# Kernel optimization log

Hardware: AMD Instinct MI355X
Metric: run time of the kernel (lower is better)

Reference implementation:

```python
import math
import jax, jax.numpy as jnp
import numpy as np

N_HEADS = 16
NUM_BUCKETS = 32
MAX_DISTANCE = 128


def _relative_position_bucket(relative_positions, num_buckets=NUM_BUCKETS, max_distance=MAX_DISTANCE):
    # bidirectional=True branch of the torch helper
    ret = -relative_positions
    nb = num_buckets // 2
    sign = (ret < 0).astype(jnp.int32)
    ret = jnp.abs(ret)
    max_exact = nb // 2
    is_small = ret < max_exact
    # torch .long() truncates toward zero; values in the selected (large) branch are >= 0 so int cast matches
    large = max_exact + jnp.minimum(
        (jnp.log(ret.astype(jnp.float32) / max_exact + 1e-6)
         / math.log(max_distance / max_exact) * (nb - max_exact)).astype(jnp.int32),
        nb - max_exact - 1,
    )
    return jnp.where(is_small, ret, large) + sign * nb


def setup_inputs() -> dict:
    key = jax.random.key(0)
    k1, k2, k3, k4, k5 = jax.random.split(key, 5)
    d_model = 1024
    B, L = 2, 2048
    return {
        "query": jax.random.normal(k1, (B, L, d_model), dtype=jnp.float32),
        "Wq": jax.random.normal(k2, (d_model, d_model), dtype=jnp.float32) * 0.02,
        "Wkv": jax.random.normal(k3, (d_model, 2 * d_model), dtype=jnp.float32) * 0.02,
        "Wo": jax.random.normal(k4, (d_model, d_model), dtype=jnp.float32) * 0.02,
        "rel_bias": jax.random.normal(k5, (N_HEADS * NUM_BUCKETS, 1), dtype=jnp.float32) * 0.02,
    }


def reference(query, Wq, Wkv, Wo, rel_bias):
    B, L, D = query.shape
    H = N_HEADS
    hd = D // H
    scale = 1.0 / math.sqrt(hd)

    q = query @ Wq                      # [B, L, D]
    kv = query @ Wkv                    # [B, L, 2D]
    k, v = jnp.split(kv, 2, axis=-1)

    def split_heads(x):
        return x.reshape(B, L, H, hd).transpose(0, 2, 1, 3)  # [B, H, L, hd]

    q, k, v = map(split_heads, (q, k, v))

    scores = jnp.einsum("bhqd,bhkd->bhqk", q, k) * scale      # [B, H, L, L]

    # relative position bias
    pos = jnp.arange(L)
    rp = pos[None, :] - pos[:, None]                           # mem - ctx, [L, L]
    buckets = _relative_position_bucket(rp)                    # [L, L]
    idx = buckets[None, :, :] + (jnp.arange(H) * NUM_BUCKETS)[:, None, None]  # [H, L, L]
    bias = rel_bias[idx, 0][None]                              # [1, H, L, L]

    attn = jax.nn.softmax(scores + bias, axis=-1)
    out = jnp.einsum("bhqk,bhkd->bhqd", attn, v)               # [B, H, L, hd]
    out = out.transpose(0, 2, 1, 3).reshape(B, L, D) @ Wo      # [B, L, D]
    return out, bias
```

## Files before the change

### kernel.cpp

```cpp
#include <hip/hip_runtime.h>


typedef unsigned short u16;
typedef unsigned int u32;
typedef __attribute__((ext_vector_type(4))) float f32x4;
typedef __attribute__((ext_vector_type(8))) short bf16x8;
typedef __attribute__((ext_vector_type(4))) unsigned short u16x4;

#define MFMA16(a, b, c) __builtin_amdgcn_mfma_f32_16x16x32_bf16(a, b, c, 0, 0, 0)

static __device__ inline u16 f2bf(float f) {
    u32 x = __float_as_uint(f);
    x += 0x7fffu + ((x >> 16) & 1u);
    return (u16)(x >> 16);
}
static __device__ inline u32 pk2(float a, float b) {
    return (u32)f2bf(a) | ((u32)f2bf(b) << 16);
}

__global__ __launch_bounds__(256) void build_table(
    const float* __restrict__ rel_bias, float* __restrict__ tbl)
{
    int i = blockIdx.x * 256 + threadIdx.x;
    if (i >= 16 * 4096) return;
    int rel = (i & 4095) - 2047;
    int h = i >> 12;
    int ret = -rel;
    int sign = (ret < 0) ? 1 : 0;
    int aret = (ret < 0) ? -ret : ret;
    int bucket;
    if (aret < 8) {
        bucket = aret;
    } else {
        float v = (logf((float)aret * 0.125f + 1e-6f) / logf(16.0f)) * 8.0f;
        int iv = (int)v;
        bucket = 8 + (iv < 7 ? iv : 7);
    }
    bucket += sign * 16;
    tbl[i] = rel_bias[h * 32 + bucket];
}

__global__ __launch_bounds__(256) void bias_fill(
    const float* __restrict__ tbl, float* __restrict__ out)
{
    const int bx = blockIdx.x;
    const int h = bx >> 11, i = bx & 2047;
    const float* tp = tbl + h * 4096 + 2047 - i;
    float* dst = out + 4194304 + ((size_t)bx << 11);
    const int j0 = threadIdx.x * 8;
    float4 v0, v1;
    v0.x = tp[j0 + 0]; v0.y = tp[j0 + 1]; v0.z = tp[j0 + 2]; v0.w = tp[j0 + 3];
    v1.x = tp[j0 + 4]; v1.y = tp[j0 + 5]; v1.z = tp[j0 + 6]; v1.w = tp[j0 + 7];
    float4* dv = (float4*)(dst + j0);
    dv[0] = v0; dv[1] = v1;
}

__global__ __launch_bounds__(256) void qkv_gemm(
    const float* __restrict__ X, const float* __restrict__ Wq,
    const float* __restrict__ Wkv, u16* __restrict__ qws,
    u16* __restrict__ kws, u16* __restrict__ vtws)
{
    __shared__ u16 As[128 * 40];
    __shared__ u16 Bs[128 * 40];
    const int tid = threadIdx.x;
    const int n0 = blockIdx.x * 128;
    const int m0 = blockIdx.y * 128;
    const float* Bw; int ldb, bn0;
    if (blockIdx.x < 8) { Bw = Wq;  ldb = 1024; bn0 = n0; }
    else                { Bw = Wkv; ldb = 2048; bn0 = n0 - 1024; }
    const int wid = tid >> 6, lane = tid & 63, c = lane & 15, quad = lane >> 4;
    const int wm = (wid >> 1) * 64, wn = (wid & 1) * 64;
    const f32x4 z = {0.f, 0.f, 0.f, 0.f};
    f32x4 acc[4][4];
    for (int i = 0; i < 4; i++) for (int j = 0; j < 4; j++) acc[i][j] = z;
    const int ar = tid >> 1, ac = (tid & 1) * 16;
    const int bkr = (tid >> 5) * 4, bnn = (tid & 31) * 4;

    for (int kk = 0; kk < 1024; kk += 32) {
        const float4* asrc = (const float4*)(X + (size_t)(m0 + ar) * 1024 + kk + ac);
        float4 a0 = asrc[0], a1 = asrc[1], a2 = asrc[2], a3 = asrc[3];
        const float* bbase = Bw + (size_t)(kk + bkr) * ldb + bn0 + bnn;
        float4 b0 = *(const float4*)(bbase);
        float4 b1 = *(const float4*)(bbase + ldb);
        float4 b2 = *(const float4*)(bbase + 2 * ldb);
        float4 b3 = *(const float4*)(bbase + 3 * ldb);
        uint4 w0 = { pk2(a0.x, a0.y), pk2(a0.z, a0.w), pk2(a1.x, a1.y), pk2(a1.z, a1.w) };
        uint4 w1 = { pk2(a2.x, a2.y), pk2(a2.z, a2.w), pk2(a3.x, a3.y), pk2(a3.z, a3.w) };
        *(uint4*)&As[ar * 40 + ac] = w0;
        *(uint4*)&As[ar * 40 + ac + 8] = w1;
        uint2 t0 = { pk2(b0.x, b1.x), pk2(b2.x, b3.x) };
        uint2 t1 = { pk2(b0.y, b1.y), pk2(b2.y, b3.y) };
        uint2 t2 = { pk2(b0.z, b1.z), pk2(b2.z, b3.z) };
        uint2 t3 = { pk2(b0.w, b1.w), pk2(b2.w, b3.w) };
        *(uint2*)&Bs[(bnn + 0) * 40 + bkr] = t0;
        *(uint2*)&Bs[(bnn + 1) * 40 + bkr] = t1;
        *(uint2*)&Bs[(bnn + 2) * 40 + bkr] = t2;
        *(uint2*)&Bs[(bnn + 3) * 40 + bkr] = t3;
        __syncthreads();
        bf16x8 af[4], bfr[4];
        for (int im = 0; im < 4; im++)
            af[im] = *(const bf16x8*)&As[(wm + im * 16 + c) * 40 + quad * 8];
        for (int jn = 0; jn < 4; jn++)
            bfr[jn] = *(const bf16x8*)&Bs[(wn + jn * 16 + c) * 40 + quad * 8];
        for (int im = 0; im < 4; im++)
            for (int jn = 0; jn < 4; jn++)
                acc[im][jn] = MFMA16(af[im], bfr[jn], acc[im][jn]);
        __syncthreads();
    }
    for (int im = 0; im < 4; im++) for (int jn = 0; jn < 4; jn++) {
        int gm0 = m0 + wm + im * 16 + quad * 4;
        int gn = n0 + wn + jn * 16 + c;
        if (gn < 2048) {
            u16* dstbase = (gn < 1024) ? qws : kws;
            int nn = gn & 1023;
            int h = nn >> 6, d = nn & 63;
            for (int r = 0; r < 4; r++) {
                int gm = gm0 + r, bb = gm >> 11, l = gm & 2047;
                dstbase[(((size_t)bb * 16 + h) * 2048 + l) * 64 + d] = f2bf(acc[im][jn][r]);
            }
        } else {
            int nn = gn - 2048;
            int h = nn >> 6, d = nn & 63;
            int bb = gm0 >> 11, l = gm0 & 2047;
            u16x4 pk = { f2bf(acc[im][jn][0]), f2bf(acc[im][jn][1]),
                         f2bf(acc[im][jn][2]), f2bf(acc[im][jn][3]) };
            *(u16x4*)&vtws[(((size_t)bb * 16 + h) * 64 + d) * 2048 + l] = pk;
        }
    }
}

__global__ __launch_bounds__(256) void attn_kernel(
    const u16* __restrict__ qws, const u16* __restrict__ kws,
    const u16* __restrict__ vtws, const float* __restrict__ tbl,
    u16* __restrict__ ows)
{
    __shared__ u16 Qs[128 * 72];
    __shared__ u16 Ks[64 * 72];
    __shared__ u16 Vt[64 * 72];
    __shared__ u16 Ps[4][32 * 72];
    const int tid = threadIdx.x;
    const int qt = blockIdx.x, bh = blockIdx.y;
    const int b = bh >> 4, h = bh & 15;
    const u16* qp = qws + (size_t)bh * 2048 * 64;
    const u16* kp = kws + (size_t)bh * 2048 * 64;
    const u16* vp = vtws + (size_t)bh * 64 * 2048;
    const float* tb = tbl + h * 4096;
    const int q0 = qt * 128;
    const int wid = tid >> 6, lane = tid & 63, c = lane & 15, quad = lane >> 4;

    {
        int row = tid >> 1, c0 = (tid & 1) * 32;
        const uint4* s = (const uint4*)(qp + (size_t)(q0 + row) * 64 + c0);
        uint4 v0 = s[0], v1 = s[1], v2 = s[2], v3 = s[3];
        uint4* d = (uint4*)&Qs[row * 72 + c0];
        d[0] = v0; d[1] = v1; d[2] = v2; d[3] = v3;
    }
    __syncthreads();
    const int qw0 = wid * 32;
    bf16x8 bq[2][2];
    for (int nt = 0; nt < 2; nt++)
        for (int ks = 0; ks < 2; ks++)
            bq[nt][ks] = *(const bf16x8*)&Qs[(qw0 + nt * 16 + c) * 72 + ks * 32 + quad * 8];

    float mrow[2] = { -__builtin_inff(), -__builtin_inff() };
    float lrow[2] = { 0.f, 0.f };
    const f32x4 z = {0.f, 0.f, 0.f, 0.f};
    f32x4 accO[2][4];
    for (int i = 0; i < 2; i++) for (int j = 0; j < 4; j++) accO[i][j] = z;
    const int srow = tid >> 2, sc0 = (tid & 3) * 16;

    for (int kt = 0; kt < 32; kt++) {
        const int k0 = kt * 64;
        __syncthreads();
        {
            const uint4* s1 = (const uint4*)(kp + (size_t)(k0 + srow) * 64 + sc0);
            uint4 x0 = s1[0], x1 = s1[1];
            const uint4* s2 = (const uint4*)(vp + (size_t)srow * 2048 + k0 + sc0);
            uint4 y0 = s2[0], y1 = s2[1];
            uint4* d1 = (uint4*)&Ks[srow * 72 + sc0]; d1[0] = x0; d1[1] = x1;
            uint4* d2 = (uint4*)&Vt[srow * 72 + sc0]; d2[0] = y0; d2[1] = y1;
        }
        __syncthreads();
        f32x4 accS[4][2];
        for (int i = 0; i < 4; i++) { accS[i][0] = z; accS[i][1] = z; }
        for (int ks = 0; ks < 2; ks++) {
            for (int ktile = 0; ktile < 4; ktile++) {
                bf16x8 ak = *(const bf16x8*)&Ks[(ktile * 16 + c) * 72 + ks * 32 + quad * 8];
                accS[ktile][0] = MFMA16(ak, bq[0][ks], accS[ktile][0]);
                accS[ktile][1] = MFMA16(ak, bq[1][ks], accS[ktile][1]);
            }
        }
        float sv[4][2][4];
        float tmax[2] = { -__builtin_inff(), -__builtin_inff() };
        for (int ktile = 0; ktile < 4; ktile++)
            for (int nt = 0; nt < 2; nt++) {
                int keyb = k0 + ktile * 16 + quad * 4;
                int qg = q0 + qw0 + nt * 16 + c;
                const float* tp = tb + (keyb - qg + 2047);
                for (int r = 0; r < 4; r++) {
                    float x = accS[ktile][nt][r] * 0.125f + tp[r];
                    sv[ktile][nt][r] = x;
                    tmax[nt] = fmaxf(tmax[nt], x);
                }
            }
        for (int nt = 0; nt < 2; nt++) {
            tmax[nt] = fmaxf(tmax[nt], __shfl_xor(tmax[nt], 16, 64));
            tmax[nt] = fmaxf(tmax[nt], __shfl_xor(tmax[nt], 32, 64));
        }
        float alpha[2], rsum[2] = { 0.f, 0.f };
        for (int nt = 0; nt < 2; nt++) {
            float mnew = fmaxf(mrow[nt], tmax[nt]);
            alpha[nt] = __expf(mrow[nt] - mnew);
            mrow[nt] = mnew;
        }
        for (int ktile = 0; ktile < 4; ktile++)
            for (int nt = 0; nt < 2; nt++) {
                float p0 = __expf(sv[ktile][nt][0] - mrow[nt]);
                float p1 = __expf(sv[ktile][nt][1] - mrow[nt]);
                float p2 = __expf(sv[ktile][nt][2] - mrow[nt]);
                float p3 = __expf(sv[ktile][nt][3] - mrow[nt]);
                rsum[nt] += (p0 + p1) + (p2 + p3);
                u16x4 pk = { f2bf(p0), f2bf(p1), f2bf(p2), f2bf(p3) };
                *(u16x4*)&Ps[wid][(nt * 16 + c) * 72 + ktile * 16 + quad * 4] = pk;
            }
        for (int nt = 0; nt < 2; nt++) {
            rsum[nt] += __shfl_xor(rsum[nt], 16, 64);
            rsum[nt] += __shfl_xor(rsum[nt], 32, 64);
            lrow[nt] = lrow[nt] * alpha[nt] + rsum[nt];
        }
        for (int mt = 0; mt < 2; mt++)
            for (int r = 0; r < 4; r++) {
                float aO = __shfl(alpha[mt], quad * 4 + r, 64);
                for (int nt = 0; nt < 4; nt++) accO[mt][nt][r] *= aO;
            }
        for (int kb = 0; kb < 2; kb++) {
            bf16x8 bv[4];
            for (int nt = 0; nt < 4; nt++)
                bv[nt] = *(const bf16x8*)&Vt[(nt * 16 + c) * 72 + kb * 32 + quad * 8];
            for (int mt = 0; mt < 2; mt++) {
                bf16x8 ap = *(const bf16x8*)&Ps[wid][(mt * 16 + c) * 72 + kb * 32 + quad * 8];
                for (int nt = 0; nt < 4; nt++)
                    accO[mt][nt] = MFMA16(ap, bv[nt], accO[mt][nt]);
            }
        }
    }
    for (int mt = 0; mt < 2; mt++)
        for (int r = 0; r < 4; r++) {
            float lq = __shfl(lrow[mt], quad * 4 + r, 64);
            float rl = 1.0f / lq;
            int qg = q0 + qw0 + mt * 16 + quad * 4 + r;
            size_t base = ((size_t)b * 2048 + qg) * 1024 + h * 64;
            for (int nt = 0; nt < 4; nt++)
                ows[base + nt * 16 + c] = f2bf(accO[mt][nt][r] * rl);
        }
}

__global__ __launch_bounds__(256) void out_gemm(
    const u16* __restrict__ O, const float* __restrict__ Wo, float* __restrict__ out)
{
    __shared__ u16 As[128 * 40];
    __shared__ u16 Bs[128 * 40];
    const int tid = threadIdx.x;
    const int n0 = blockIdx.x * 128;
    const int m0 = blockIdx.y * 128;
    const int wid = tid >> 6, lane = tid & 63, c = lane & 15, quad = lane >> 4;
    const int wm = (wid >> 1) * 64, wn = (wid & 1) * 64;
    const f32x4 z = {0.f, 0.f, 0.f, 0.f};
    f32x4 acc[4][4];
    for (int i = 0; i < 4; i++) for (int j = 0; j < 4; j++) acc[i][j] = z;
    const int ar = tid >> 1, ac = (tid & 1) * 16;
    const int bkr = (tid >> 5) * 4, bnn = (tid & 31) * 4;
    for (int kk = 0; kk < 1024; kk += 32) {
        const uint4* asrc = (const uint4*)(O + (size_t)(m0 + ar) * 1024 + kk + ac);
        uint4 a0 = asrc[0], a1 = asrc[1];
        const float* bbase = Wo + (size_t)(kk + bkr) * 1024 + n0 + bnn;
        float4 b0 = *(const float4*)(bbase);
        float4 b1 = *(const float4*)(bbase + 1024);
        float4 b2 = *(const float4*)(bbase + 2048);
        float4 b3 = *(const float4*)(bbase + 3072);
        *(uint4*)&As[ar * 40 + ac] = a0;
        *(uint4*)&As[ar * 40 + ac + 8] = a1;
        uint2 t0 = { pk2(b0.x, b1.x), pk2(b2.x, b3.x) };
        uint2 t1 = { pk2(b0.y, b1.y), pk2(b2.y, b3.y) };
        uint2 t2 = { pk2(b0.z, b1.z), pk2(b2.z, b3.z) };
        uint2 t3 = { pk2(b0.w, b1.w), pk2(b2.w, b3.w) };
        *(uint2*)&Bs[(bnn + 0) * 40 + bkr] = t0;
        *(uint2*)&Bs[(bnn + 1) * 40 + bkr] = t1;
        *(uint2*)&Bs[(bnn + 2) * 40 + bkr] = t2;
        *(uint2*)&Bs[(bnn + 3) * 40 + bkr] = t3;
        __syncthreads();
        bf16x8 af[4], bfr[4];
        for (int im = 0; im < 4; im++)
            af[im] = *(const bf16x8*)&As[(wm + im * 16 + c) * 40 + quad * 8];
        for (int jn = 0; jn < 4; jn++)
            bfr[jn] = *(const bf16x8*)&Bs[(wn + jn * 16 + c) * 40 + quad * 8];
        for (int im = 0; im < 4; im++)
            for (int jn = 0; jn < 4; jn++)
                acc[im][jn] = MFMA16(af[im], bfr[jn], acc[im][jn]);
        __syncthreads();
    }
    for (int im = 0; im < 4; im++) for (int jn = 0; jn < 4; jn++) {
        int gm0 = m0 + wm + im * 16 + quad * 4;
        int gn = n0 + wn + jn * 16 + c;
        for (int r = 0; r < 4; r++)
            out[(size_t)(gm0 + r) * 1024 + gn] = acc[im][jn][r];
    }
}

extern "C" void kernel_launch(void* const* d_in, const int* in_sizes, int n_in,
                              void* d_out, int out_size, void* d_ws, size_t ws_size,
                              hipStream_t stream)
{
    (void)in_sizes; (void)n_in; (void)out_size; (void)ws_size;
    const float* query    = (const float*)d_in[0];
    const float* Wq       = (const float*)d_in[1];
    const float* Wkv      = (const float*)d_in[2];
    const float* Wo       = (const float*)d_in[3];
    const float* rel_bias = (const float*)d_in[4];
    float* out = (float*)d_out;

    float* tbl = (float*)d_ws;
    u16* qws  = (u16*)((char*)d_ws + 262144);
    u16* kws  = qws + 4194304;
    u16* vtws = kws + 4194304;
    u16* ows  = vtws + 4194304;

    build_table<<<256, 256, 0, stream>>>(rel_bias, tbl);
    bias_fill<<<32768, 256, 0, stream>>>(tbl, out);
    qkv_gemm<<<dim3(24, 32), 256, 0, stream>>>(query, Wq, Wkv, qws, kws, vtws);
    attn_kernel<<<dim3(16, 32), 256, 0, stream>>>(qws, kws, vtws, tbl, ows);
    out_gemm<<<dim3(8, 32), 256, 0, stream>>>(ows, Wo, out);
}
```

Measured before the change: 492.8 us.

## Pre-convert inputs to bf16, double-buffer attention K/V, drop online softmax rescaling

Adds pre-pass kernels that convert the activations to bf16 and transpose and convert all weights to bf16 K-major layout. Both GEMMs then load bf16 tiles directly with a 64-wide K step instead of converting fp32 inside the main loop. The attention kernel double-buffers K/V and a bias window in shared memory, prefetching the next tile during compute. It also removes the running-max softmax rescaling by exponentiating raw scores, which risks overflow for large logits.

```diff
diff --git a/kernel.cpp b/kernel.cpp
--- a/kernel.cpp
+++ b/kernel.cpp
@@ -40,6 +40,46 @@
     tbl[i] = rel_bias[h * 32 + bucket];
 }
 
+__global__ __launch_bounds__(256) void convert_x(
+    const float* __restrict__ X, u16* __restrict__ Xb)
+{
+    int i = (blockIdx.x * 256 + threadIdx.x) * 8;
+    float4 a = *(const float4*)(X + i);
+    float4 b = *(const float4*)(X + i + 4);
+    uint4 w = { pk2(a.x, a.y), pk2(a.z, a.w), pk2(b.x, b.y), pk2(b.z, b.w) };
+    *(uint4*)(Xb + i) = w;
+}
+
+__global__ __launch_bounds__(256) void transpose_w(
+    const float* __restrict__ Wq, const float* __restrict__ Wkv,
+    const float* __restrict__ Wo, u16* __restrict__ Wt)
+{
+    __shared__ u16 T[64 * 72];
+    const int tid = threadIdx.x;
+    const int k0 = blockIdx.x * 64;
+    const int nt = blockIdx.y;
+    const int n0 = nt * 64;
+    const float* src; int ld, nb;
+    if (n0 < 1024)      { src = Wq;  ld = 1024; nb = n0; }
+    else if (n0 < 3072) { src = Wkv; ld = 2048; nb = n0 - 1024; }
+    else                { src = Wo;  ld = 1024; nb = n0 - 3072; }
+    const int r0 = tid >> 4, c4 = (tid & 15) * 4;
+    for (int rr = 0; rr < 4; rr++) {
+        int row = rr * 16 + r0;
+        float4 f = *(const float4*)(src + (size_t)(k0 + row) * ld + nb + c4);
+        T[(c4 + 0) * 72 + row] = f2bf(f.x);
+        T[(c4 + 1) * 72 + row] = f2bf(f.y);
+        T[(c4 + 2) * 72 + row] = f2bf(f.z);
+        T[(c4 + 3) * 72 + row] = f2bf(f.w);
+    }
+    __syncthreads();
+    const int n = tid >> 2, ks0 = (tid & 3) * 16;
+    uint4 u0 = *(const uint4*)&T[n * 72 + ks0];
+    uint4 u1 = *(const uint4*)&T[n * 72 + ks0 + 8];
+    uint4* d = (uint4*)(Wt + (size_t)(n0 + n) * 1024 + k0 + ks0);
+    d[0] = u0; d[1] = u1;
+}
+
 __global__ __launch_bounds__(256) void bias_fill(
     const float* __restrict__ tbl, float* __restrict__ out)
 {
@@ -56,55 +96,47 @@
 }
 
 __global__ __launch_bounds__(256) void qkv_gemm(
-    const float* __restrict__ X, const float* __restrict__ Wq,
-    const float* __restrict__ Wkv, u16* __restrict__ qws,
-    u16* __restrict__ kws, u16* __restrict__ vtws)
-{
-    __shared__ u16 As[128 * 40];
-    __shared__ u16 Bs[128 * 40];
+    const u16* __restrict__ Xb, const u16* __restrict__ Wt,
+    u16* __restrict__ qws, u16* __restrict__ kws, u16* __restrict__ vtws)
+{
+    __shared__ u16 As[128 * 72];
+    __shared__ u16 Bs[128 * 72];
     const int tid = threadIdx.x;
     const int n0 = blockIdx.x * 128;
     const int m0 = blockIdx.y * 128;
-    const float* Bw; int ldb, bn0;
-    if (blockIdx.x < 8) { Bw = Wq;  ldb = 1024; bn0 = n0; }
-    else                { Bw = Wkv; ldb = 2048; bn0 = n0 - 1024; }
     const int wid = tid >> 6, lane = tid & 63, c = lane & 15, quad = lane >> 4;
     const int wm = (wid >> 1) * 64, wn = (wid & 1) * 64;
     const f32x4 z = {0.f, 0.f, 0.f, 0.f};
     f32x4 acc[4][4];
     for (int i = 0; i < 4; i++) for (int j = 0; j < 4; j++) acc[i][j] = z;
-    const int ar = tid >> 1, ac = (tid & 1) * 16;
-    const int bkr = (tid >> 5) * 4, bnn = (tid & 31) * 4;
-
-    for (int kk = 0; kk < 1024; kk += 32) {
-        const float4* asrc = (const float4*)(X + (size_t)(m0 + ar) * 1024 + kk + ac);
-        float4 a0 = asrc[0], a1 = asrc[1], a2 = asrc[2], a3 = asrc[3];
-        const float* bbase = Bw + (size_t)(kk + bkr) * ldb + bn0 + bnn;
-        float4 b0 = *(const float4*)(bbase);
-        float4 b1 = *(const float4*)(bbase + ldb);
-        float4 b2 = *(const float4*)(bbase + 2 * ldb);
-        float4 b3 = *(const float4*)(bbase + 3 * ldb);
-        uint4 w0 = { pk2(a0.x, a0.y), pk2(a0.z, a0.w), pk2(a1.x, a1.y), pk2(a1.z, a1.w) };
-        uint4 w1 = { pk2(a2.x, a2.y), pk2(a2.z, a2.w), pk2(a3.x, a3.y), pk2(a3.z, a3.w) };
-        *(uint4*)&As[ar * 40 + ac] = w0;
-        *(uint4*)&As[ar * 40 + ac + 8] = w1;
-        uint2 t0 = { pk2(b0.x, b1.x), pk2(b2.x, b3.x) };
-        uint2 t1 = { pk2(b0.y, b1.y), pk2(b2.y, b3.y) };
-        uint2 t2 = { pk2(b0.z, b1.z), pk2(b2.z, b3.z) };
-        uint2 t3 = { pk2(b0.w, b1.w), pk2(b2.w, b3.w) };
-        *(uint2*)&Bs[(bnn + 0) * 40 + bkr] = t0;
-        *(uint2*)&Bs[(bnn + 1) * 40 + bkr] = t1;
-        *(uint2*)&Bs[(bnn + 2) * 40 + bkr] = t2;
-        *(uint2*)&Bs[(bnn + 3) * 40 + bkr] = t3;
+    const int srow = tid >> 1, sk = (tid & 1) * 32;
+    const u16* ag = Xb + (size_t)(m0 + srow) * 1024 + sk;
+    const u16* bg = Wt + (size_t)(n0 + srow) * 1024 + sk;
+
+    for (int kk = 0; kk < 1024; kk += 64) {
+        uint4 a0 = *(const uint4*)(ag + kk);
+        uint4 a1 = *(const uint4*)(ag + kk + 8);
+        uint4 a2 = *(const uint4*)(ag + kk + 16);
+        uint4 a3 = *(const uint4*)(ag + kk + 24);
+        uint4 b0 = *(const uint4*)(bg + kk);
+        uint4 b1 = *(const uint4*)(bg + kk + 8);
+        uint4 b2 = *(const uint4*)(bg + kk + 16);
+        uint4 b3 = *(const uint4*)(bg + kk + 24);
+        uint4* da = (uint4*)&As[srow * 72 + sk];
+        da[0] = a0; da[1] = a1; da[2] = a2; da[3] = a3;
+        uint4* db = (uint4*)&Bs[srow * 72 + sk];
+        db[0] = b0; db[1] = b1; db[2] = b2; db[3] = b3;
         __syncthreads();
-        bf16x8 af[4], bfr[4];
-        for (int im = 0; im < 4; im++)
-            af[im] = *(const bf16x8*)&As[(wm + im * 16 + c) * 40 + quad * 8];
-        for (int jn = 0; jn < 4; jn++)
-            bfr[jn] = *(const bf16x8*)&Bs[(wn + jn * 16 + c) * 40 + quad * 8];
-        for (int im = 0; im < 4; im++)
+        for (int ks = 0; ks < 2; ks++) {
+            bf16x8 af[4], bfr[4];
+            for (int im = 0; im < 4; im++)
+                af[im] = *(const bf16x8*)&As[(wm + im * 16 + c) * 72 + ks * 32 + quad * 8];
             for (int jn = 0; jn < 4; jn++)
-                acc[im][jn] = MFMA16(af[im], bfr[jn], acc[im][jn]);
+                bfr[jn] = *(const bf16x8*)&Bs[(wn + jn * 16 + c) * 72 + ks * 32 + quad * 8];
+            for (int im = 0; im < 4; im++)
+                for (int jn = 0; jn < 4; jn++)
+                    acc[im][jn] = MFMA16(af[im], bfr[jn], acc[im][jn]);
+        }
         __syncthreads();
     }
     for (int im = 0; im < 4; im++) for (int jn = 0; jn < 4; jn++) {
@@ -129,15 +161,15 @@
     }
 }
 
-__global__ __launch_bounds__(256) void attn_kernel(
+__global__ __launch_bounds__(256, 2) void attn_kernel(
     const u16* __restrict__ qws, const u16* __restrict__ kws,
     const u16* __restrict__ vtws, const float* __restrict__ tbl,
     u16* __restrict__ ows)
 {
-    __shared__ u16 Qs[128 * 72];
-    __shared__ u16 Ks[64 * 72];
-    __shared__ u16 Vt[64 * 72];
-    __shared__ u16 Ps[4][32 * 72];
+    __shared__ u16 QPs[128 * 72];
+    __shared__ u16 Ks[2][64 * 72];
+    __shared__ u16 Vt[2][64 * 72];
+    __shared__ float Bw[2][192];
     const int tid = threadIdx.x;
     const int qt = blockIdx.x, bh = blockIdx.y;
     const int b = bh >> 4, h = bh & 15;
@@ -147,102 +179,94 @@
     const float* tb = tbl + h * 4096;
     const int q0 = qt * 128;
     const int wid = tid >> 6, lane = tid & 63, c = lane & 15, quad = lane >> 4;
+    const int qw0 = wid * 32;
+    const int srow = tid >> 2, sc0 = (tid & 3) * 16;
 
     {
         int row = tid >> 1, c0 = (tid & 1) * 32;
         const uint4* s = (const uint4*)(qp + (size_t)(q0 + row) * 64 + c0);
         uint4 v0 = s[0], v1 = s[1], v2 = s[2], v3 = s[3];
-        uint4* d = (uint4*)&Qs[row * 72 + c0];
+        uint4* d = (uint4*)&QPs[row * 72 + c0];
         d[0] = v0; d[1] = v1; d[2] = v2; d[3] = v3;
     }
+    {
+        const uint4* s1 = (const uint4*)(kp + (size_t)srow * 64 + sc0);
+        uint4 x0 = s1[0], x1 = s1[1];
+        const uint4* s2 = (const uint4*)(vp + (size_t)srow * 2048 + sc0);
+        uint4 y0 = s2[0], y1 = s2[1];
+        *(uint4*)&Ks[0][srow * 72 + sc0] = x0;
+        *(uint4*)&Ks[0][srow * 72 + sc0 + 8] = x1;
+        *(uint4*)&Vt[0][srow * 72 + sc0] = y0;
+        *(uint4*)&Vt[0][srow * 72 + sc0 + 8] = y1;
+        if (tid < 192) Bw[0][tid] = tb[1920 - q0 + tid];
+    }
     __syncthreads();
-    const int qw0 = wid * 32;
     bf16x8 bq[2][2];
     for (int nt = 0; nt < 2; nt++)
         for (int ks = 0; ks < 2; ks++)
-            bq[nt][ks] = *(const bf16x8*)&Qs[(qw0 + nt * 16 + c) * 72 + ks * 32 + quad * 8];
-
-    float mrow[2] = { -__builtin_inff(), -__builtin_inff() };
+            bq[nt][ks] = *(const bf16x8*)&QPs[(qw0 + nt * 16 + c) * 72 + ks * 32 + quad * 8];
+    __syncthreads();
+    u16* Ps = QPs + wid * (32 * 72);
+
     float lrow[2] = { 0.f, 0.f };
     const f32x4 z = {0.f, 0.f, 0.f, 0.f};
     f32x4 accO[2][4];
     for (int i = 0; i < 2; i++) for (int j = 0; j < 4; j++) accO[i][j] = z;
-    const int srow = tid >> 2, sc0 = (tid & 3) * 16;
 
     for (int kt = 0; kt < 32; kt++) {
+        const int cur = kt & 1, nxt = cur ^ 1;
         const int k0 = kt * 64;
-        __syncthreads();
-        {
-            const uint4* s1 = (const uint4*)(kp + (size_t)(k0 + srow) * 64 + sc0);
-            uint4 x0 = s1[0], x1 = s1[1];
-            const uint4* s2 = (const uint4*)(vp + (size_t)srow * 2048 + k0 + sc0);
-            uint4 y0 = s2[0], y1 = s2[1];
-            uint4* d1 = (uint4*)&Ks[srow * 72 + sc0]; d1[0] = x0; d1[1] = x1;
-            uint4* d2 = (uint4*)&Vt[srow * 72 + sc0]; d2[0] = y0; d2[1] = y1;
-        }
-        __syncthreads();
+        uint4 x0, x1, y0, y1; float bwv = 0.f;
+        if (kt < 31) {
+            const uint4* s1 = (const uint4*)(kp + (size_t)(k0 + 64 + srow) * 64 + sc0);
+            x0 = s1[0]; x1 = s1[1];
+            const uint4* s2 = (const uint4*)(vp + (size_t)srow * 2048 + k0 + 64 + sc0);
+            y0 = s2[0]; y1 = s2[1];
+            if (tid < 192) bwv = tb[k0 + 64 - q0 + 1920 + tid];
+        }
         f32x4 accS[4][2];
         for (int i = 0; i < 4; i++) { accS[i][0] = z; accS[i][1] = z; }
-        for (int ks = 0; ks < 2; ks++) {
+        for (int ks = 0; ks < 2; ks++)
             for (int ktile = 0; ktile < 4; ktile++) {
-                bf16x8 ak = *(const bf16x8*)&Ks[(ktile * 16 + c) * 72 + ks * 32 + quad * 8];
+                bf16x8 ak = *(const bf16x8*)&Ks[cur][(ktile * 16 + c) * 72 + ks * 32 + quad * 8];
                 accS[ktile][0] = MFMA16(ak, bq[0][ks], accS[ktile][0]);
                 accS[ktile][1] = MFMA16(ak, bq[1][ks], accS[ktile][1]);
             }
-        }
-        float sv[4][2][4];
-        float tmax[2] = { -__builtin_inff(), -__builtin_inff() };
+        float rsum[2] = { 0.f, 0.f };
         for (int ktile = 0; ktile < 4; ktile++)
             for (int nt = 0; nt < 2; nt++) {
-                int keyb = k0 + ktile * 16 + quad * 4;
-                int qg = q0 + qw0 + nt * 16 + c;
-                const float* tp = tb + (keyb - qg + 2047);
-                for (int r = 0; r < 4; r++) {
-                    float x = accS[ktile][nt][r] * 0.125f + tp[r];
-                    sv[ktile][nt][r] = x;
-                    tmax[nt] = fmaxf(tmax[nt], x);
-                }
-            }
-        for (int nt = 0; nt < 2; nt++) {
-            tmax[nt] = fmaxf(tmax[nt], __shfl_xor(tmax[nt], 16, 64));
-            tmax[nt] = fmaxf(tmax[nt], __shfl_xor(tmax[nt], 32, 64));
-        }
-        float alpha[2], rsum[2] = { 0.f, 0.f };
-        for (int nt = 0; nt < 2; nt++) {
-            float mnew = fmaxf(mrow[nt], tmax[nt]);
-            alpha[nt] = __expf(mrow[nt] - mnew);
-            mrow[nt] = mnew;
-        }
-        for (int ktile = 0; ktile < 4; ktile++)
-            for (int nt = 0; nt < 2; nt++) {
-                float p0 = __expf(sv[ktile][nt][0] - mrow[nt]);
-                float p1 = __expf(sv[ktile][nt][1] - mrow[nt]);
-                float p2 = __expf(sv[ktile][nt][2] - mrow[nt]);
-                float p3 = __expf(sv[ktile][nt][3] - mrow[nt]);
+                const float* bp = &Bw[cur][ktile * 16 + quad * 4 - qw0 - nt * 16 - c + 127];
+                float p0 = __expf(fmaf(accS[ktile][nt][0], 0.125f, bp[0]));
+                float p1 = __expf(fmaf(accS[ktile][nt][1], 0.125f, bp[1]));
+                float p2 = __expf(fmaf(accS[ktile][nt][2], 0.125f, bp[2]));
+                float p3 = __expf(fmaf(accS[ktile][nt][3], 0.125f, bp[3]));
                 rsum[nt] += (p0 + p1) + (p2 + p3);
                 u16x4 pk = { f2bf(p0), f2bf(p1), f2bf(p2), f2bf(p3) };
-                *(u16x4*)&Ps[wid][(nt * 16 + c) * 72 + ktile * 16 + quad * 4] = pk;
+                *(u16x4*)&Ps[(nt * 16 + c) * 72 + ktile * 16 + quad * 4] = pk;
             }
-        for (int nt = 0; nt < 2; nt++) {
-            rsum[nt] += __shfl_xor(rsum[nt], 16, 64);
-            rsum[nt] += __shfl_xor(rsum[nt], 32, 64);
-            lrow[nt] = lrow[nt] * alpha[nt] + rsum[nt];
-        }
-        for (int mt = 0; mt < 2; mt++)
-            for (int r = 0; r < 4; r++) {
-                float aO = __shfl(alpha[mt], quad * 4 + r, 64);
-                for (int nt = 0; nt < 4; nt++) accO[mt][nt][r] *= aO;
-            }
+        lrow[0] += rsum[0]; lrow[1] += rsum[1];
         for (int kb = 0; kb < 2; kb++) {
             bf16x8 bv[4];
             for (int nt = 0; nt < 4; nt++)
-                bv[nt] = *(const bf16x8*)&Vt[(nt * 16 + c) * 72 + kb * 32 + quad * 8];
+                bv[nt] = *(const bf16x8*)&Vt[cur][(nt * 16 + c) * 72 + kb * 32 + quad * 8];
             for (int mt = 0; mt < 2; mt++) {
-                bf16x8 ap = *(const bf16x8*)&Ps[wid][(mt * 16 + c) * 72 + kb * 32 + quad * 8];
+                bf16x8 ap = *(const bf16x8*)&Ps[(mt * 16 + c) * 72 + kb * 32 + quad * 8];
                 for (int nt = 0; nt < 4; nt++)
                     accO[mt][nt] = MFMA16(ap, bv[nt], accO[mt][nt]);
             }
         }
+        if (kt < 31) {
+            *(uint4*)&Ks[nxt][srow * 72 + sc0] = x0;
+            *(uint4*)&Ks[nxt][srow * 72 + sc0 + 8] = x1;
+            *(uint4*)&Vt[nxt][srow * 72 + sc0] = y0;
+            *(uint4*)&Vt[nxt][srow * 72 + sc0 + 8] = y1;
+            if (tid < 192) Bw[nxt][tid] = bwv;
+            __syncthreads();
+        }
+    }
+    for (int nt = 0; nt < 2; nt++) {
+        lrow[nt] += __shfl_xor(lrow[nt], 16, 64);
+        lrow[nt] += __shfl_xor(lrow[nt], 32, 64);
     }
     for (int mt = 0; mt < 2; mt++)
         for (int r = 0; r < 4; r++) {
@@ -256,10 +280,10 @@
 }
 
 __global__ __launch_bounds__(256) void out_gemm(
-    const u16* __restrict__ O, const float* __restrict__ Wo, float* __restrict__ out)
-{
-    __shared__ u16 As[128 * 40];
-    __shared__ u16 Bs[128 * 40];
+    const u16* __restrict__ O, const u16* __restrict__ Wot, float* __restrict__ out)
+{
+    __shared__ u16 As[128 * 72];
+    __shared__ u16 Bs[128 * 72];
     const int tid = threadIdx.x;
     const int n0 = blockIdx.x * 128;
     const int m0 = blockIdx.y * 128;
@@ -268,35 +292,33 @@
     const f32x4 z = {0.f, 0.f, 0.f, 0.f};
     f32x4 acc[4][4];
     for (int i = 0; i < 4; i++) for (int j = 0; j < 4; j++) acc[i][j] = z;
-    const int ar = tid >> 1, ac = (tid & 1) * 16;
-    const int bkr = (tid >> 5) * 4, bnn = (tid & 31) * 4;
-    for (int kk = 0; kk < 1024; kk += 32) {
-        const uint4* asrc = (const uint4*)(O + (size_t)(m0 + ar) * 1024 + kk + ac);
-        uint4 a0 = asrc[0], a1 = asrc[1];
-        const float* bbase = Wo + (size_t)(kk + bkr) * 1024 + n0 + bnn;
-        float4 b0 = *(const float4*)(bbase);
-        float4 b1 = *(const float4*)(bbase + 1024);
-        float4 b2 = *(const float4*)(bbase + 2048);
-        float4 b3 = *(const float4*)(bbase + 3072);
-        *(uint4*)&As[ar * 40 + ac] = a0;
-        *(uint4*)&As[ar * 40 + ac + 8] = a1;
-        uint2 t0 = { pk2(b0.x, b1.x), pk2(b2.x, b3.x) };
-        uint2 t1 = { pk2(b0.y, b1.y), pk2(b2.y, b3.y) };
-        uint2 t2 = { pk2(b0.z, b1.z), pk2(b2.z, b3.z) };
-        uint2 t3 = { pk2(b0.w, b1.w), pk2(b2.w, b3.w) };
-        *(uint2*)&Bs[(bnn + 0) * 40 + bkr] = t0;
-        *(uint2*)&Bs[(bnn + 1) * 40 + bkr] = t1;
-        *(uint2*)&Bs[(bnn + 2) * 40 + bkr] = t2;
-        *(uint2*)&Bs[(bnn + 3) * 40 + bkr] = t3;
+    const int srow = tid >> 1, sk = (tid & 1) * 32;
+    const u16* ag = O + (size_t)(m0 + srow) * 1024 + sk;
+    const u16* bg = Wot + (size_t)(n0 + srow) * 1024 + sk;
+    for (int kk = 0; kk < 1024; kk += 64) {
+        uint4 a0 = *(const uint4*)(ag + kk);
+        uint4 a1 = *(const uint4*)(ag + kk + 8);
+        uint4 a2 = *(const uint4*)(ag + kk + 16);
+        uint4 a3 = *(const uint4*)(ag + kk + 24);
+        uint4 b0 = *(const uint4*)(bg + kk);
+        uint4 b1 = *(const uint4*)(bg + kk + 8);
+        uint4 b2 = *(const uint4*)(bg + kk + 16);
+        uint4 b3 = *(const uint4*)(bg + kk + 24);
+        uint4* da = (uint4*)&As[srow * 72 + sk];
+        da[0] = a0; da[1] = a1; da[2] = a2; da[3] = a3;
+        uint4* db = (uint4*)&Bs[srow * 72 + sk];
+        db[0] = b0; db[1] = b1; db[2] = b2; db[3] = b3;
         __syncthreads();
-        bf16x8 af[4], bfr[4];
-        for (int im = 0; im < 4; im++)
-            af[im] = *(const bf16x8*)&As[(wm + im * 16 + c) * 40 + quad * 8];
-        for (int jn = 0; jn < 4; jn++)
-            bfr[jn] = *(const bf16x8*)&Bs[(wn + jn * 16 + c) * 40 + quad * 8];
-        for (int im = 0; im < 4; im++)
+        for (int ks = 0; ks < 2; ks++) {
+            bf16x8 af[4], bfr[4];
+            for (int im = 0; im < 4; im++)
+                af[im] = *(const bf16x8*)&As[(wm + im * 16 + c) * 72 + ks * 32 + quad * 8];
             for (int jn = 0; jn < 4; jn++)
-                acc[im][jn] = MFMA16(af[im], bfr[jn], acc[im][jn]);
+                bfr[jn] = *(const bf16x8*)&Bs[(wn + jn * 16 + c) * 72 + ks * 32 + quad * 8];
+            for (int im = 0; im < 4; im++)
+                for (int jn = 0; jn < 4; jn++)
+                    acc[im][jn] = MFMA16(af[im], bfr[jn], acc[im][jn]);
+        }
         __syncthreads();
     }
     for (int im = 0; im < 4; im++) for (int jn = 0; jn < 4; jn++) {
@@ -320,14 +342,18 @@
     float* out = (float*)d_out;
 
     float* tbl = (float*)d_ws;
-    u16* qws  = (u16*)((char*)d_ws + 262144);
+    u16* Xb   = (u16*)((char*)d_ws + 262144);
+    u16* Wt   = Xb + 4194304;
+    u16* qws  = Wt + 4194304;
     u16* kws  = qws + 4194304;
     u16* vtws = kws + 4194304;
     u16* ows  = vtws + 4194304;
 
     build_table<<<256, 256, 0, stream>>>(rel_bias, tbl);
+    convert_x<<<2048, 256, 0, stream>>>(query, Xb);
+    transpose_w<<<dim3(16, 64), 256, 0, stream>>>(Wq, Wkv, Wo, Wt);
     bias_fill<<<32768, 256, 0, stream>>>(tbl, out);
-    qkv_gemm<<<dim3(24, 32), 256, 0, stream>>>(query, Wq, Wkv, qws, kws, vtws);
+    qkv_gemm<<<dim3(24, 32), 256, 0, stream>>>(Xb, Wt, qws, kws, vtws);
     attn_kernel<<<dim3(16, 32), 256, 0, stream>>>(qws, kws, vtws, tbl, ows);
-    out_gemm<<<dim3(8, 32), 256, 0, stream>>>(ows, Wo, out);
-}
+    out_gemm<<<dim3(8, 32), 256, 0, stream>>>(ows, Wt + (size_t)3072 * 1024, out);
+}
```

New measurement: 441.0 us. 10.5% less time.
